# Kernel tuning notes

Measured on AMD Instinct MI355X. Metric: run time of the kernel, lower is better.

## Reference

```python
import jax, jax.numpy as jnp
import numpy as np

N_SRC0, N_DST0 = 400000, 100000
N_DST1 = 25000


def _graph_conv(x_src, src, dst, n_dst, W, b):
    # DGL GraphConv, norm='both': h_v = d_in(v)^-1/2 * sum_{u->v} d_out(u)^-1/2 * x_u @ W + b
    ones = jnp.ones(src.shape[0], dtype=x_src.dtype)
    out_deg = jax.ops.segment_sum(ones, src, num_segments=x_src.shape[0])
    in_deg = jax.ops.segment_sum(ones, dst, num_segments=n_dst)
    cs = jnp.where(out_deg > 0, out_deg ** -0.5, 0.0).astype(x_src.dtype)
    cd = jnp.where(in_deg > 0, in_deg ** -0.5, 0.0).astype(x_src.dtype)
    msg = (x_src * cs[:, None])[src]                      # [E, d_in] gather
    agg = jax.ops.segment_sum(msg, dst, num_segments=n_dst)  # [n_dst, d_in] scatter-add
    return (agg * cd[:, None]) @ W + b


def setup_inputs() -> dict:
    key = jax.random.key(0)
    ks = jax.random.split(key, 8)
    E0, E1 = 3200000, 800000
    return {
        "x": jax.random.normal(ks[0], (N_SRC0, 128), dtype=jnp.float32),
        "src0": jax.random.randint(ks[1], (E0,), 0, N_SRC0, dtype=jnp.int32),
        "dst0": jax.random.randint(ks[2], (E0,), 0, N_DST0, dtype=jnp.int32),
        "src1": jax.random.randint(ks[3], (E1,), 0, N_DST0, dtype=jnp.int32),
        "dst1": jax.random.randint(ks[4], (E1,), 0, N_DST1, dtype=jnp.int32),
        "W0": jax.random.normal(ks[5], (128, 256), dtype=jnp.float32) * (128 ** -0.5),
        "b0": jnp.zeros((256,), dtype=jnp.float32),
        "W1": jax.random.normal(ks[6], (256, 64), dtype=jnp.float32) * (256 ** -0.5),
        "b1": jnp.zeros((64,), dtype=jnp.float32),
    }


def reference(x, src0, dst0, src1, dst1, W0, b0, W1, b1):
    h = jax.nn.relu(_graph_conv(x, src0, dst0, N_DST0, W0, b0))   # [N_DST0, 256]
    h = jax.nn.relu(_graph_conv(h, src1, dst1, N_DST1, W1, b1))   # [N_DST1, 64]
    return h
```

## Files before the change

### kernel.cpp

```cpp
#include <hip/hip_runtime.h>
#include <hip/hip_bf16.h>
#include <hip/hip_fp16.h>
#include <stdint.h>

#define N_SRC0 400000
#define N_DST0 100000
#define N_DST1 25000

#define SH_D0 9
#define NK_D0 196
#define SH_S0 9
#define NK_S0 782
#define SH_D1 8
#define NK_D1 98
#define SH_S1 9
#define NK_S1 196
#define NB0 1024
#define NB1 256

#define BH_D0 0
#define BH_S0 (NK_D0 * NB0)
#define BH_D1 (BH_S0 + NK_S0 * NB0)
#define BH_S1 (BH_D1 + NK_D1 * NB1)
#define BH_TOT (BH_S1 + NK_S1 * NB1)

typedef __attribute__((ext_vector_type(8))) short short8;
typedef __attribute__((ext_vector_type(4))) float f32x4;

__device__ __forceinline__ unsigned short f2bf(float f) {
    __hip_bfloat16 h = __float2bfloat16(f);
    union { __hip_bfloat16 h; unsigned short u; } c;
    c.h = h;
    return c.u;
}
__device__ __forceinline__ uint32_t packbf2(float a, float b) {
    return (uint32_t)f2bf(a) | ((uint32_t)f2bf(b) << 16);
}
__device__ __forceinline__ __half2 u2h2(uint32_t u) {
    return __builtin_bit_cast(__half2, u);
}

__device__ __forceinline__ void hist_body(
        const int* __restrict__ src, const int* __restrict__ dst, int n,
        int sshift, int snb, int dshift, int dnb, int NB, int blk,
        int* __restrict__ bhd, int* __restrict__ bhs, int* h) {
    for (int i = threadIdx.x; i < dnb + snb; i += 256) h[i] = 0;
    __syncthreads();
    const int per = (n + NB - 1) / NB;
    const int b = blk * per;
    const int e = min(b + per, n);
    for (int i = b + threadIdx.x; i < e; i += 256) {
        atomicAdd(&h[dst[i] >> dshift], 1);
        atomicAdd(&h[dnb + (src[i] >> sshift)], 1);
    }
    __syncthreads();
    for (int i = threadIdx.x; i < dnb; i += 256) bhd[(size_t)i * NB + blk] = h[i];
    for (int i = threadIdx.x; i < snb; i += 256) bhs[(size_t)i * NB + blk] = h[dnb + i];
}

__global__ __launch_bounds__(256) void hist_fused(
        const int* __restrict__ src0, const int* __restrict__ dst0, int E0,
        const int* __restrict__ src1, const int* __restrict__ dst1, int E1,
        int* __restrict__ bh) {
    extern __shared__ int h[];
    if (blockIdx.x < NB0)
        hist_body(src0, dst0, E0, SH_S0, NK_S0, SH_D0, NK_D0, NB0, blockIdx.x,
                  bh + BH_D0, bh + BH_S0, h);
    else
        hist_body(src1, dst1, E1, SH_S1, NK_S1, SH_D1, NK_D1, NB1, blockIdx.x - NB0,
                  bh + BH_D1, bh + BH_S1, h);
}

#define SCAN_ITEMS 8
#define SCAN_TILE 2048

__global__ __launch_bounds__(256) void scan1_kernel(
        const int* __restrict__ in, int* __restrict__ out,
        int* __restrict__ sums, int n) {
    __shared__ int lds[256];
    const int tid = threadIdx.x;
    const int base = blockIdx.x * SCAN_TILE + tid * SCAN_ITEMS;
    int v[SCAN_ITEMS];
    int run = 0;
    #pragma unroll
    for (int i = 0; i < SCAN_ITEMS; ++i) {
        int t = (base + i < n) ? in[base + i] : 0;
        v[i] = run;
        run += t;
    }
    lds[tid] = run;
    __syncthreads();
    int incl = run;
    for (int off = 1; off < 256; off <<= 1) {
        int u = (tid >= off) ? lds[tid - off] : 0;
        __syncthreads();
        incl += u;
        lds[tid] = incl;
        __syncthreads();
    }
    if (tid == 255) sums[blockIdx.x] = incl;
    int excl = incl - run;
    #pragma unroll
    for (int i = 0; i < SCAN_ITEMS; ++i)
        if (base + i < n) out[base + i] = excl + v[i];
}

__global__ __launch_bounds__(256) void scan2_kernel(int* __restrict__ sums, int nb) {
    __shared__ int lds[256];
    const int tid = threadIdx.x;
    const int base = tid * 4;
    int v[4];
    int run = 0;
    #pragma unroll
    for (int i = 0; i < 4; ++i) {
        int t = (base + i < nb) ? sums[base + i] : 0;
        v[i] = run;
        run += t;
    }
    lds[tid] = run;
    __syncthreads();
    int incl = run;
    for (int off = 1; off < 256; off <<= 1) {
        int u = (tid >= off) ? lds[tid - off] : 0;
        __syncthreads();
        incl += u;
        lds[tid] = incl;
        __syncthreads();
    }
    int excl = incl - run;
    #pragma unroll
    for (int i = 0; i < 4; ++i)
        if (base + i < nb) sums[base + i] = excl + v[i];
}

__global__ void scan3_kernel(int* __restrict__ out, const int* __restrict__ sums, int n) {
    int i = blockIdx.x * blockDim.x + threadIdx.x;
    if (i < n) out[i] += sums[i / SCAN_TILE];
}

__device__ __forceinline__ void scat_body(
        const int* __restrict__ src, const int* __restrict__ dst, int n,
        int sshift, int snb, int dshift, int dnb, int NB, int blk, int ksh,
        const int* __restrict__ bhd, const int* __restrict__ bhs,
        uint32_t* __restrict__ stg, int* cur) {
    for (int i = threadIdx.x; i < dnb; i += 256) cur[i] = bhd[(size_t)i * NB + blk];
    for (int i = threadIdx.x; i < snb; i += 256) cur[dnb + i] = bhs[(size_t)i * NB + blk];
    __syncthreads();
    const int per = (n + NB - 1) / NB;
    const int b = blk * per;
    const int e = min(b + per, n);
    const int dmask = (1 << dshift) - 1;
    for (int i = b + threadIdx.x; i < e; i += 256) {
        int s = src[i], d = dst[i];
        int pd = atomicAdd(&cur[d >> dshift], 1);
        stg[pd] = ((uint32_t)(d & dmask) << ksh) | (uint32_t)s;
        int ps = atomicAdd(&cur[dnb + (s >> sshift)], 1);
        stg[ps] = (uint32_t)s;
    }
}

__global__ __launch_bounds__(256) void scat_fused(
        const int* __restrict__ src0, const int* __restrict__ dst0, int E0,
        const int* __restrict__ src1, const int* __restrict__ dst1, int E1,
        const int* __restrict__ bh, uint32_t* __restrict__ stg) {
    extern __shared__ int cur[];
    if (blockIdx.x < NB0)
        scat_body(src0, dst0, E0, SH_S0, NK_S0, SH_D0, NK_D0, NB0, blockIdx.x, 19,
                  bh + BH_D0, bh + BH_S0, stg, cur);
    else
        scat_body(src1, dst1, E1, SH_S1, NK_S1, SH_D1, NK_D1, NB1, blockIdx.x - NB0, 17,
                  bh + BH_D1, bh + BH_S1, stg, cur);
}

__device__ __forceinline__ void fine_csr_body(
        const uint32_t* __restrict__ stg, const int* __restrict__ bht,
        int NB, int shift, int ksh, int nbins, int total, int rel, int nbkt, int k,
        int* __restrict__ off, int* __restrict__ esrc, int* fine, int* part) {
    const int fb = 1 << shift;
    const int base = bht[(size_t)k * NB];
    const int end = (k + 1 < nbkt) ? bht[(size_t)(k + 1) * NB] : total;
    const int gb = k << shift;
    const int t = threadIdx.x;
    const uint32_t mask = (1u << ksh) - 1;
    for (int i = t; i < fb; i += 256) fine[i] = 0;
    __syncthreads();
    for (int i = base + t; i < end; i += 256)
        atomicAdd(&fine[stg[i] >> ksh], 1);
    __syncthreads();
    int a0 = (2 * t < fb) ? fine[2 * t] : 0;
    int a1 = (2 * t + 1 < fb) ? fine[2 * t + 1] : 0;
    part[t] = a0 + a1;
    __syncthreads();
    int incl = part[t];
    for (int o = 1; o < 256; o <<= 1) {
        int u = (t >= o) ? part[t - o] : 0;
        __syncthreads();
        incl += u;
        part[t] = incl;
        __syncthreads();
    }
    int excl = incl - (a0 + a1);
    if (2 * t < fb) fine[2 * t] = excl;
    if (2 * t + 1 < fb) fine[2 * t + 1] = excl + a0;
    __syncthreads();
    const int rb = base - rel;
    for (int i = t; i < fb; i += 256) {
        int g = gb + i;
        if (g < nbins) off[g] = rb + fine[i];
    }
    if (k == nbkt - 1 && t == 0) off[nbins] = total - rel;
    __syncthreads();
    for (int i = base + t; i < end; i += 256) {
        uint32_t v = stg[i];
        int p = atomicAdd(&fine[v >> ksh], 1);
        esrc[rb + p] = (int)(v & mask);
    }
}

__device__ __forceinline__ void fine_deg_body(
        const uint32_t* __restrict__ stg, const int* __restrict__ bht,
        int NB, int shift, int nbins, int total, int nbkt, int k,
        float* __restrict__ csf, int* fine) {
    const int fb = 1 << shift;
    const int base = bht[(size_t)k * NB];
    const int end = (k + 1 < nbkt) ? bht[(size_t)(k + 1) * NB] : total;
    const int gb = k << shift;
    for (int i = threadIdx.x; i < fb; i += 256) fine[i] = 0;
    __syncthreads();
    for (int i = base + threadIdx.x; i < end; i += 256)
        atomicAdd(&fine[(int)stg[i] - gb], 1);
    __syncthreads();
    for (int i = threadIdx.x; i < fb; i += 256) {
        int g = gb + i;
        if (g < nbins) {
            int c = fine[i];
            csf[g] = c > 0 ? rsqrtf((float)c) : 0.f;
        }
    }
}

__global__ __launch_bounds__(256) void fine_fused(
        const uint32_t* __restrict__ stg, const int* __restrict__ bh,
        int E0, int E1,
        int* __restrict__ off0, int* __restrict__ esrc0,
        int* __restrict__ off1, int* __restrict__ esrc1,
        float* __restrict__ cs0, float* __restrict__ cs1) {
    __shared__ int fine[512];
    __shared__ int part[256];
    int kb = blockIdx.x;
    if (kb < NK_D0) {
        fine_csr_body(stg, bh + BH_D0, NB0, SH_D0, 19, N_DST0, E0, 0, NK_D0, kb,
                      off0, esrc0, fine, part);
        return;
    }
    kb -= NK_D0;
    if (kb < NK_S0) {
        fine_deg_body(stg, bh + BH_S0, NB0, SH_S0, N_SRC0, 2 * E0, NK_S0, kb,
                      cs0, fine);
        return;
    }
    kb -= NK_S0;
    if (kb < NK_D1) {
        fine_csr_body(stg, bh + BH_D1, NB1, SH_D1, 17, N_DST1, 2 * E0 + E1, 2 * E0, NK_D1, kb,
                      off1, esrc1, fine, part);
        return;
    }
    kb -= NK_D1;
    fine_deg_body(stg, bh + BH_S1, NB1, SH_S1, N_DST0, 2 * E0 + 2 * E1, NK_S1, kb,
                  cs1, fine);
}

__global__ __launch_bounds__(256) void prescale_kernel(
        const float4* __restrict__ x4, const float* __restrict__ cs,
        uint2* __restrict__ xs) {
    int id = blockIdx.x * 256 + threadIdx.x;
    int row = id >> 5;
    float c = cs[row];
    float4 v = x4[id];
    uint2 o;
    o.x = __builtin_bit_cast(uint32_t, __floats2half2_rn(v.x * c, v.y * c));
    o.y = __builtin_bit_cast(uint32_t, __floats2half2_rn(v.z * c, v.w * c));
    xs[id] = o;
}

__global__ __launch_bounds__(256) void packw_fused(
        const float* __restrict__ W0, const float* __restrict__ W1,
        unsigned short* __restrict__ W0p, unsigned short* __restrict__ W1p) {
    int blk = blockIdx.x;
    if (blk < 128) {
        int id = blk * 256 + threadIdx.x;
        int kk = id & 31, n2 = (id >> 5) & 255, kt = id >> 13;
        W0p[id] = f2bf(W0[(kt * 32 + kk) * 256 + n2]);
    } else {
        int id = (blk - 128) * 256 + threadIdx.x;
        int kk = id & 31, n2 = (id >> 5) & 63, kt = id >> 11;
        W1p[id] = f2bf(W1[(kt * 32 + kk) * 64 + n2]);
    }
}

__global__ __launch_bounds__(256) void agg0_kernel(
        const uint32_t* __restrict__ xs, const int* __restrict__ esrc,
        const int* __restrict__ off, uint32_t* __restrict__ aggb) {
    const int row = blockIdx.x * 4 + (threadIdx.x >> 6);
    const int t = threadIdx.x & 63;
    const int b = off[row], e = off[row + 1];
    const __half2 z = __builtin_bit_cast(__half2, 0u);
    __half2 a0 = z, a1 = z, a2 = z, a3 = z, a4 = z, a5 = z, a6 = z, a7 = z;
    int i = b;
    for (; i + 7 < e; i += 8) {
        int s0 = esrc[i],     s1 = esrc[i + 1], s2 = esrc[i + 2], s3 = esrc[i + 3];
        int s4 = esrc[i + 4], s5 = esrc[i + 5], s6 = esrc[i + 6], s7 = esrc[i + 7];
        a0 = __hadd2(a0, u2h2(xs[(size_t)s0 * 64 + t]));
        a1 = __hadd2(a1, u2h2(xs[(size_t)s1 * 64 + t]));
        a2 = __hadd2(a2, u2h2(xs[(size_t)s2 * 64 + t]));
        a3 = __hadd2(a3, u2h2(xs[(size_t)s3 * 64 + t]));
        a4 = __hadd2(a4, u2h2(xs[(size_t)s4 * 64 + t]));
        a5 = __hadd2(a5, u2h2(xs[(size_t)s5 * 64 + t]));
        a6 = __hadd2(a6, u2h2(xs[(size_t)s6 * 64 + t]));
        a7 = __hadd2(a7, u2h2(xs[(size_t)s7 * 64 + t]));
    }
    for (; i < e; ++i)
        a0 = __hadd2(a0, u2h2(xs[(size_t)esrc[i] * 64 + t]));
    __half2 s = __hadd2(__hadd2(__hadd2(a0, a1), __hadd2(a2, a3)),
                        __hadd2(__hadd2(a4, a5), __hadd2(a6, a7)));
    float cd = (e > b) ? rsqrtf((float)(e - b)) : 0.f;
    aggb[(size_t)row * 64 + t] = packbf2(__low2float(s) * cd, __high2float(s) * cd);
}

__global__ __launch_bounds__(256) void gemm01_mfma(
        const short* __restrict__ A,
        const short* __restrict__ B0p,
        const float* __restrict__ bias0,
        const short* __restrict__ B1p,
        const float* __restrict__ cs1,
        __half* __restrict__ Y) {
    __shared__ short hs[32][272];
    const int w = threadIdx.x >> 6;
    const int l = threadIdx.x & 63;
    const int rbase = blockIdx.x * 32;
    const int lr = l & 15;
    const int lk = (l >> 4) * 8;
    const int orow0 = (l >> 4) * 4;

    {
        const int cbase = w * 64;
        f32x4 acc[2][4] = {};
        #pragma unroll
        for (int kt = 0; kt < 4; ++kt) {
            short8 a[2], b[4];
            #pragma unroll
            for (int rt = 0; rt < 2; ++rt)
                a[rt] = *(const short8*)(A + (size_t)(rbase + rt * 16 + lr) * 128 + kt * 32 + lk);
            #pragma unroll
            for (int ct = 0; ct < 4; ++ct)
                b[ct] = *(const short8*)(B0p + (size_t)(kt * 256 + cbase + ct * 16 + lr) * 32 + lk);
            #pragma unroll
            for (int rt = 0; rt < 2; ++rt)
                #pragma unroll
                for (int ct = 0; ct < 4; ++ct)
                    acc[rt][ct] = __builtin_amdgcn_mfma_f32_16x16x32_bf16(a[rt], b[ct], acc[rt][ct], 0, 0, 0);
        }
        #pragma unroll
        for (int rt = 0; rt < 2; ++rt) {
            #pragma unroll
            for (int ct = 0; ct < 4; ++ct) {
                int col = cbase + ct * 16 + lr;
                float bv = bias0[col];
                #pragma unroll
                for (int j = 0; j < 4; ++j)
                    hs[rt * 16 + orow0 + j][col] = (short)f2bf(fmaxf(acc[rt][ct][j] + bv, 0.f));
            }
        }
    }
    __syncthreads();

    {
        f32x4 acc2[2] = {};
        #pragma unroll
        for (int kt = 0; kt < 8; ++kt) {
            short8 b1 = *(const short8*)(B1p + (size_t)(kt * 64 + w * 16 + lr) * 32 + lk);
            #pragma unroll
            for (int rt = 0; rt < 2; ++rt) {
                short8 av = *(const short8*)(&hs[rt * 16 + lr][kt * 32 + lk]);
                acc2[rt] = __builtin_amdgcn_mfma_f32_16x16x32_bf16(av, b1, acc2[rt], 0, 0, 0);
            }
        }
        #pragma unroll
        for (int rt = 0; rt < 2; ++rt) {
            #pragma unroll
            for (int j = 0; j < 4; ++j) {
                int row = rbase + rt * 16 + orow0 + j;
                float c = cs1[row];
                Y[(size_t)row * 64 + w * 16 + lr] = __float2half(acc2[rt][j] * c);
            }
        }
    }
}

__global__ __launch_bounds__(256) void agg1_kernel(
        const uint2* __restrict__ y2, const int* __restrict__ esrc,
        const int* __restrict__ off, const float* __restrict__ bias,
        float* __restrict__ out, int nrows) {
    int row = blockIdx.x * 16 + (threadIdx.x >> 4);
    int t = threadIdx.x & 15;
    if (row >= nrows) return;
    int b = off[row], e = off[row + 1];
    const __half2 z = __builtin_bit_cast(__half2, 0u);
    __half2 aA0 = z, aA1 = z, aB0 = z, aB1 = z;
    int i = b;
    for (; i + 8 <= e; i += 8) {
        #pragma unroll
        for (int k = 0; k < 8; k += 2) {
            int s0 = esrc[i + k], s1 = esrc[i + k + 1];
            uint2 v0 = y2[(size_t)s0 * 16 + t];
            uint2 v1 = y2[(size_t)s1 * 16 + t];
            aA0 = __hadd2(aA0, u2h2(v0.x));
            aA1 = __hadd2(aA1, u2h2(v0.y));
            aB0 = __hadd2(aB0, u2h2(v1.x));
            aB1 = __hadd2(aB1, u2h2(v1.y));
        }
    }
    for (; i < e; ++i) {
        uint2 v = y2[(size_t)esrc[i] * 16 + t];
        aA0 = __hadd2(aA0, u2h2(v.x));
        aA1 = __hadd2(aA1, u2h2(v.y));
    }
    float cd = (e > b) ? rsqrtf((float)(e - b)) : 0.f;
    __half2 s0 = __hadd2(aA0, aB0), s1 = __hadd2(aA1, aB1);
    float4 bv = *(const float4*)(bias + t * 4);
    float4 o;
    o.x = fmaxf(__low2float(s0) * cd + bv.x, 0.f);
    o.y = fmaxf(__high2float(s0) * cd + bv.y, 0.f);
    o.z = fmaxf(__low2float(s1) * cd + bv.z, 0.f);
    o.w = fmaxf(__high2float(s1) * cd + bv.w, 0.f);
    *(float4*)(out + (size_t)row * 64 + t * 4) = o;
}

extern "C" void kernel_launch(void* const* d_in, const int* in_sizes, int n_in,
                              void* d_out, int out_size, void* d_ws, size_t ws_size,
                              hipStream_t stream) {
    const float* x    = (const float*)d_in[0];
    const int*   src0 = (const int*)d_in[1];
    const int*   dst0 = (const int*)d_in[2];
    const int*   src1 = (const int*)d_in[3];
    const int*   dst1 = (const int*)d_in[4];
    const float* W0   = (const float*)d_in[5];
    const float* b0   = (const float*)d_in[6];
    const float* W1   = (const float*)d_in[7];
    const float* b1   = (const float*)d_in[8];
    float* out = (float*)d_out;

    const int E0 = in_sizes[1];
    const int E1 = in_sizes[3];

    char* p = (char*)d_ws;
    auto alloc = [&](size_t bytes) {
        char* r = p;
        p += (bytes + 511) & ~(size_t)511;
        return r;
    };
    int*   bh    = (int*)alloc((size_t)BH_TOT * 4);
    int*   sums  = (int*)alloc(1024 * 4);
    int*   off0  = (int*)alloc((size_t)(N_DST0 + 1) * 4);
    int*   off1  = (int*)alloc((size_t)(N_DST1 + 1) * 4);
    float* cs0   = (float*)alloc((size_t)N_SRC0 * 4);
    float* cs1   = (float*)alloc((size_t)N_DST0 * 4);
    int*   esrc0 = (int*)alloc((size_t)E0 * 4);
    int*   esrc1 = (int*)alloc((size_t)E1 * 4);
    unsigned short* W0p = (unsigned short*)alloc((size_t)32768 * 2);
    unsigned short* W1p = (unsigned short*)alloc((size_t)16384 * 2);
    size_t bigA = (size_t)N_SRC0 * 128 * 2;
    size_t bigB = (size_t)N_DST0 * 128 * 2;
    size_t bigStg = (size_t)(2 * E0 + 2 * E1) * 4;
    size_t bigSz = bigA + bigB;
    if (bigStg > bigSz) bigSz = bigStg;
    char* big = alloc(bigSz);

    uint32_t* stg  = (uint32_t*)big;
    uint2*    xs   = (uint2*)big;
    __half*   y1b  = (__half*)big;
    uint32_t* aggb = (uint32_t*)(big + bigA);

    hist_fused<<<NB0 + NB1, 256, (NK_D0 + NK_S0) * 4, stream>>>(
        src0, dst0, E0, src1, dst1, E1, bh);
    const int nsb = (BH_TOT + SCAN_TILE - 1) / SCAN_TILE;
    scan1_kernel<<<nsb, 256, 0, stream>>>(bh, bh, sums, BH_TOT);
    scan2_kernel<<<1, 256, 0, stream>>>(sums, nsb);
    scan3_kernel<<<(BH_TOT + 255) / 256, 256, 0, stream>>>(bh, sums, BH_TOT);
    scat_fused<<<NB0 + NB1, 256, (NK_D0 + NK_S0) * 4, stream>>>(
        src0, dst0, E0, src1, dst1, E1, bh, stg);
    fine_fused<<<NK_D0 + NK_S0 + NK_D1 + NK_S1, 256, 0, stream>>>(
        stg, bh, E0, E1, off0, esrc0, off1, esrc1, cs0, cs1);

    packw_fused<<<192, 256, 0, stream>>>(W0, W1, W0p, W1p);
    prescale_kernel<<<N_SRC0 * 32 / 256, 256, 0, stream>>>((const float4*)x, cs0, xs);

    agg0_kernel<<<N_DST0 / 4, 256, 0, stream>>>(
        (const uint32_t*)xs, esrc0, off0, aggb);

    gemm01_mfma<<<N_DST0 / 32, 256, 0, stream>>>(
        (const short*)aggb, (const short*)W0p, b0, (const short*)W1p, cs1, y1b);

    agg1_kernel<<<(N_DST1 + 15) / 16, 256, 0, stream>>>(
        (const uint2*)y1b, esrc1, off1, b1, out, N_DST1);
}
```

Measured before the change: 397.6 us.

## Fold weight packing into fine_fused, widen agg0 gather unroll, shrink LDS padding

Weight packing into bf16 now runs as 192 extra blocks of fine_fused, which removes one kernel launch. The agg0 gather loop is unrolled to 16 independent loads and accumulators, with a 4-wide tail and 32-bit index arithmetic, so more memory requests are in flight per wave. The GEMM shared-memory row padding changes from 272 to 264 shorts. That padding change can alter bank conflicts, and the wider unroll raises register pressure.

```diff
diff --git a/kernel.cpp b/kernel.cpp
--- a/kernel.cpp
+++ b/kernel.cpp
@@ -244,7 +244,9 @@
         int E0, int E1,
         int* __restrict__ off0, int* __restrict__ esrc0,
         int* __restrict__ off1, int* __restrict__ esrc1,
-        float* __restrict__ cs0, float* __restrict__ cs1) {
+        float* __restrict__ cs0, float* __restrict__ cs1,
+        const float* __restrict__ W0, const float* __restrict__ W1,
+        unsigned short* __restrict__ W0p, unsigned short* __restrict__ W1p) {
     __shared__ int fine[512];
     __shared__ int part[256];
     int kb = blockIdx.x;
@@ -266,8 +268,21 @@
         return;
     }
     kb -= NK_D1;
-    fine_deg_body(stg, bh + BH_S1, NB1, SH_S1, N_DST0, 2 * E0 + 2 * E1, NK_S1, kb,
-                  cs1, fine);
+    if (kb < NK_S1) {
+        fine_deg_body(stg, bh + BH_S1, NB1, SH_S1, N_DST0, 2 * E0 + 2 * E1, NK_S1, kb,
+                      cs1, fine);
+        return;
+    }
+    kb -= NK_S1;
+    if (kb < 128) {
+        int id = kb * 256 + threadIdx.x;
+        int kk = id & 31, n2 = (id >> 5) & 255, kt = id >> 13;
+        W0p[id] = f2bf(W0[(kt * 32 + kk) * 256 + n2]);
+    } else {
+        int id = (kb - 128) * 256 + threadIdx.x;
+        int kk = id & 31, n2 = (id >> 5) & 63, kt = id >> 11;
+        W1p[id] = f2bf(W1[(kt * 32 + kk) * 64 + n2]);
+    }
 }
 
 __global__ __launch_bounds__(256) void prescale_kernel(
@@ -283,46 +298,38 @@
     xs[id] = o;
 }
 
-__global__ __launch_bounds__(256) void packw_fused(
-        const float* __restrict__ W0, const float* __restrict__ W1,
-        unsigned short* __restrict__ W0p, unsigned short* __restrict__ W1p) {
-    int blk = blockIdx.x;
-    if (blk < 128) {
-        int id = blk * 256 + threadIdx.x;
-        int kk = id & 31, n2 = (id >> 5) & 255, kt = id >> 13;
-        W0p[id] = f2bf(W0[(kt * 32 + kk) * 256 + n2]);
-    } else {
-        int id = (blk - 128) * 256 + threadIdx.x;
-        int kk = id & 31, n2 = (id >> 5) & 63, kt = id >> 11;
-        W1p[id] = f2bf(W1[(kt * 32 + kk) * 64 + n2]);
-    }
-}
-
 __global__ __launch_bounds__(256) void agg0_kernel(
         const uint32_t* __restrict__ xs, const int* __restrict__ esrc,
         const int* __restrict__ off, uint32_t* __restrict__ aggb) {
     const int row = blockIdx.x * 4 + (threadIdx.x >> 6);
-    const int t = threadIdx.x & 63;
+    const uint32_t t = threadIdx.x & 63;
     const int b = off[row], e = off[row + 1];
     const __half2 z = __builtin_bit_cast(__half2, 0u);
-    __half2 a0 = z, a1 = z, a2 = z, a3 = z, a4 = z, a5 = z, a6 = z, a7 = z;
+    __half2 a[16];
+    #pragma unroll
+    for (int k = 0; k < 16; ++k) a[k] = z;
     int i = b;
-    for (; i + 7 < e; i += 8) {
-        int s0 = esrc[i],     s1 = esrc[i + 1], s2 = esrc[i + 2], s3 = esrc[i + 3];
-        int s4 = esrc[i + 4], s5 = esrc[i + 5], s6 = esrc[i + 6], s7 = esrc[i + 7];
-        a0 = __hadd2(a0, u2h2(xs[(size_t)s0 * 64 + t]));
-        a1 = __hadd2(a1, u2h2(xs[(size_t)s1 * 64 + t]));
-        a2 = __hadd2(a2, u2h2(xs[(size_t)s2 * 64 + t]));
-        a3 = __hadd2(a3, u2h2(xs[(size_t)s3 * 64 + t]));
-        a4 = __hadd2(a4, u2h2(xs[(size_t)s4 * 64 + t]));
-        a5 = __hadd2(a5, u2h2(xs[(size_t)s5 * 64 + t]));
-        a6 = __hadd2(a6, u2h2(xs[(size_t)s6 * 64 + t]));
-        a7 = __hadd2(a7, u2h2(xs[(size_t)s7 * 64 + t]));
+    for (; i + 15 < e; i += 16) {
+        uint32_t idx[16];
+        #pragma unroll
+        for (int k = 0; k < 16; ++k)
+            idx[k] = ((uint32_t)esrc[i + k] << 6) + t;
+        #pragma unroll
+        for (int k = 0; k < 16; ++k)
+            a[k] = __hadd2(a[k], u2h2(xs[idx[k]]));
+    }
+    for (; i + 3 < e; i += 4) {
+        #pragma unroll
+        for (int k = 0; k < 4; ++k)
+            a[k] = __hadd2(a[k], u2h2(xs[((uint32_t)esrc[i + k] << 6) + t]));
     }
     for (; i < e; ++i)
-        a0 = __hadd2(a0, u2h2(xs[(size_t)esrc[i] * 64 + t]));
-    __half2 s = __hadd2(__hadd2(__hadd2(a0, a1), __hadd2(a2, a3)),
-                        __hadd2(__hadd2(a4, a5), __hadd2(a6, a7)));
+        a[0] = __hadd2(a[0], u2h2(xs[((uint32_t)esrc[i] << 6) + t]));
+    #pragma unroll
+    for (int k = 0; k < 8; ++k) a[k] = __hadd2(a[k], a[k + 8]);
+    #pragma unroll
+    for (int k = 0; k < 4; ++k) a[k] = __hadd2(a[k], a[k + 4]);
+    __half2 s = __hadd2(__hadd2(a[0], a[1]), __hadd2(a[2], a[3]));
     float cd = (e > b) ? rsqrtf((float)(e - b)) : 0.f;
     aggb[(size_t)row * 64 + t] = packbf2(__low2float(s) * cd, __high2float(s) * cd);
 }
@@ -334,7 +341,7 @@
         const short* __restrict__ B1p,
         const float* __restrict__ cs1,
         __half* __restrict__ Y) {
-    __shared__ short hs[32][272];
+    __shared__ short hs[32][264];
     const int w = threadIdx.x >> 6;
     const int l = threadIdx.x & 63;
     const int rbase = blockIdx.x * 32;
@@ -489,10 +496,9 @@
     scan3_kernel<<<(BH_TOT + 255) / 256, 256, 0, stream>>>(bh, sums, BH_TOT);
     scat_fused<<<NB0 + NB1, 256, (NK_D0 + NK_S0) * 4, stream>>>(
         src0, dst0, E0, src1, dst1, E1, bh, stg);
-    fine_fused<<<NK_D0 + NK_S0 + NK_D1 + NK_S1, 256, 0, stream>>>(
-        stg, bh, E0, E1, off0, esrc0, off1, esrc1, cs0, cs1);
-
-    packw_fused<<<192, 256, 0, stream>>>(W0, W1, W0p, W1p);
+    fine_fused<<<NK_D0 + NK_S0 + NK_D1 + NK_S1 + 192, 256, 0, stream>>>(
+        stg, bh, E0, E1, off0, esrc0, off1, esrc1, cs0, cs1, W0, W1, W0p, W1p);
+
     prescale_kernel<<<N_SRC0 * 32 / 256, 256, 0, stream>>>((const float4*)x, cs0, xs);
 
     agg0_kernel<<<N_DST0 / 4, 256, 0, stream>>>(
```

Result: faster. 388.9 us (-2.2%).
